# Performance work log

Hardware: AMD Instinct MI355X
Metric: run time of the kernel (lower is better)

## Reference

```python
import jax, jax.numpy as jnp
import numpy as np

D_MODEL = 1024
N_HEADS = 16
D_V = D_MODEL // N_HEADS  # 64


def setup_inputs() -> dict:
    key = jax.random.key(0)
    k1, k2, k3, k4, k5, k6 = jax.random.split(key, 6)
    N, L = 2, 2048
    return {
        "queries": jax.random.normal(k1, (N, L, D_MODEL), jnp.float32),
        "keys": jax.random.normal(k2, (N, L, D_MODEL), jnp.float32),
        "values": jax.random.normal(k3, (N, L, D_MODEL), jnp.float32),
        # key-padding mask, 0 = masked out (broadcast over heads and queries)
        "mask": jax.random.randint(k4, (N, 1, 1, L), 0, 2).astype(jnp.int32),
        # torch nn.Linear(d_model, d_model): weight [out, in], bias [out]
        "fc_w": jax.random.normal(k5, (D_MODEL, D_MODEL), jnp.float32) / np.sqrt(D_MODEL).astype(np.float32),
        "fc_b": jax.random.normal(k6, (D_MODEL,), jnp.float32) * 0.01,
    }


def reference(queries, keys, values, mask, fc_w, fc_b):
    N, Lq, _ = queries.shape
    Lk = keys.shape[1]
    # NOTE: the source defines Q/K/V Linear layers but never applies them in forward.
    q = queries.reshape(N, Lq, N_HEADS, D_V).transpose(0, 2, 1, 3)  # [N,H,Lq,Dv]
    k = keys.reshape(N, Lk, N_HEADS, D_V)                            # [N,Lk,H,Dv]
    v = values.reshape(N, Lk, N_HEADS, D_V)                          # [N,Lk,H,Dv]
    energy = jnp.einsum('nhqd,nkhd->nhqk', q, k)                     # QK^T
    energy = jnp.where(mask == 0, -jnp.inf, energy)                  # masked_fill
    # faithful to source: scale by sqrt(d_model), applied after masking
    attn = jax.nn.softmax(energy / jnp.sqrt(jnp.float32(D_MODEL)), axis=-1)
    out = jnp.einsum('nhqk,nkhd->nqhd', attn, v).reshape(N, Lq, N_HEADS * D_V)
    return out @ fc_w.T + fc_b
```

## Files before the change

kernel.cpp:

```cpp
#include <hip/hip_runtime.h>
#include <hip/hip_bf16.h>

#define SEQL 2048
#define DMODEL 1024

typedef short bf16x8 __attribute__((ext_vector_type(8)));
typedef short bf16x4 __attribute__((ext_vector_type(4)));
typedef float f32x4 __attribute__((ext_vector_type(4)));
typedef unsigned short u16;

__device__ __forceinline__ u16 f2bf(float f) {
    union { float f; unsigned u; } v; v.f = f;
    unsigned r = v.u + 0x7FFFu + ((v.u >> 16) & 1u);
    return (u16)(r >> 16);
}

#define TSTR 66

__global__ __launch_bounds__(256) void pack_all(
    const float* __restrict__ kg, const float* __restrict__ wg,
    const float* __restrict__ vg, const int* __restrict__ mg,
    u16* __restrict__ kb, u16* __restrict__ wb, u16* __restrict__ vtb,
    float* __restrict__ maskf)
{
    __shared__ __align__(16) u16 T[64 * TSTR];
    const int b = blockIdx.x, t = threadIdx.x;
    u16 o[8];
    if (b < 2048) {
        const int e0 = (b * 256 + t) * 8;
        const int n = e0 >> 21, rem = e0 & ((1 << 21) - 1);
        const int s = rem >> 10, dm = rem & 1023, h = dm >> 6, d = dm & 63;
        const float4 x0 = *(const float4*)(kg + e0);
        const float4 x1 = *(const float4*)(kg + e0 + 4);
        o[0]=f2bf(x0.x); o[1]=f2bf(x0.y); o[2]=f2bf(x0.z); o[3]=f2bf(x0.w);
        o[4]=f2bf(x1.x); o[5]=f2bf(x1.y); o[6]=f2bf(x1.z); o[7]=f2bf(x1.w);
        *(bf16x8*)(kb + ((((size_t)n * 16 + h) * 2048 + s) * 64 + d)) = *(bf16x8*)o;
    } else if (b < 2560) {
        const int e0 = ((b - 2048) * 256 + t) * 8;
        const float4 x0 = *(const float4*)(wg + e0);
        const float4 x1 = *(const float4*)(wg + e0 + 4);
        o[0]=f2bf(x0.x); o[1]=f2bf(x0.y); o[2]=f2bf(x0.z); o[3]=f2bf(x0.w);
        o[4]=f2bf(x1.x); o[5]=f2bf(x1.y); o[6]=f2bf(x1.z); o[7]=f2bf(x1.w);
        *(bf16x8*)(wb + e0) = *(bf16x8*)o;
    } else if (b < 3584) {
        const int bb = b - 2560;
        const int st = bb & 31, h = (bb >> 5) & 15, n = bb >> 9;
        {
            const int s = t >> 2, d0 = (t & 3) * 16;
            const float* src = vg + ((size_t)(n * SEQL + st * 64 + s) * DMODEL) + h * 64 + d0;
            u16 w16[16];
            #pragma unroll
            for (int j = 0; j < 16; ++j) w16[j] = f2bf(src[j]);
            *(bf16x8*)&T[s * TSTR + d0]     = *(bf16x8*)&w16[0];
            *(bf16x8*)&T[s * TSTR + d0 + 8] = *(bf16x8*)&w16[8];
        }
        __syncthreads();
        {
            const int d = t >> 2, k0 = (t & 3) * 16;
            u16 w16[16];
            #pragma unroll
            for (int j = 0; j < 16; ++j) w16[j] = T[(k0 + j) * TSTR + d];
            u16* dst = vtb + ((size_t)((n * 16 + h) * 64 + d) * SEQL) + st * 64 + k0;
            *(bf16x8*)dst       = *(bf16x8*)&w16[0];
            *(bf16x8*)(dst + 8) = *(bf16x8*)&w16[8];
        }
    } else {
        #pragma unroll
        for (int i = 0; i < 16; ++i) {
            const int idx = t * 16 + i;
            maskf[idx] = mg[idx] ? 0.0f : -1.0e5f;
        }
    }
}

#define KSTR 66
#define VSTR 66
#define PT 66
#define OSPLIT 4194304
#define LSPLIT 65536

template<int NSPLIT>
__global__ __launch_bounds__(256) void attn_kernel(
    const float* __restrict__ qg, const u16* __restrict__ kb,
    const u16* __restrict__ vtb, const float* __restrict__ maskf,
    u16* __restrict__ xb, float* __restrict__ opart, float* __restrict__ lpart)
{
    __shared__ __align__(16) u16 K_lds[64 * KSTR];
    __shared__ __align__(16) u16 Vt_lds[64 * VSTR];
    __shared__ __align__(16) u16 P_lds[128 * PT];

    const int blk = blockIdx.x;
    const int qblk = blk & 15;
    const int h = (blk >> 4) & 15;
    const int n = (blk >> 8) & 1;
    const int split = blk >> 9;
    const int tid = threadIdx.x;
    const int wave = tid >> 6, lane = tid & 63;
    const int lrow = lane & 15, quad = lane >> 4;
    const int q0 = qblk * 128;

    bf16x8 qf[2][2];
    #pragma unroll
    for (int qi = 0; qi < 2; ++qi) {
        const float* qp = qg + ((size_t)(n * SEQL + q0 + wave * 32 + qi * 16 + lrow) * DMODEL) + h * 64 + quad * 8;
        #pragma unroll
        for (int f = 0; f < 2; ++f) {
            const float4 a = *(const float4*)(qp + f * 32);
            const float4 c = *(const float4*)(qp + f * 32 + 4);
            u16* dst = (u16*)&qf[qi][f];
            dst[0]=f2bf(a.x); dst[1]=f2bf(a.y); dst[2]=f2bf(a.z); dst[3]=f2bf(a.w);
            dst[4]=f2bf(c.x); dst[5]=f2bf(c.y); dst[6]=f2bf(c.z); dst[7]=f2bf(c.w);
        }
    }

    bf16x8 onesf;
    #pragma unroll
    for (int j = 0; j < 8; ++j) ((u16*)&onesf)[j] = 0x3F80;

    f32x4 oacc[2][4];
    f32x4 lacc[2];
    #pragma unroll
    for (int qi = 0; qi < 2; ++qi) {
        lacc[qi] = (f32x4){0.f, 0.f, 0.f, 0.f};
        #pragma unroll
        for (int t4 = 0; t4 < 4; ++t4) oacc[qi][t4] = (f32x4){0.f, 0.f, 0.f, 0.f};
    }

    const u16* ksrc0 = kb  + ((size_t)(n * 16 + h) * SEQL) * 64;
    const u16* vsrc0 = vtb + ((size_t)(n * 16 + h) * 64) * SEQL;
    const float* mrow = maskf + n * SEQL;

    const int ktlo = split * (32 / NSPLIT);
    const int kthi = ktlo + (32 / NSPLIT);

    for (int kt = ktlo; kt < kthi; ++kt) {
        __syncthreads();
        {
            const u16* ks = ksrc0 + (size_t)kt * 64 * 64;
            const u16* vs = vsrc0 + kt * 64;
            #pragma unroll
            for (int i = 0; i < 2; ++i) {
                const int c = tid + i * 256;
                const int r = c >> 3, e0 = (c & 7) * 8;
                *(bf16x8*)&K_lds[r * KSTR + e0]  = *(const bf16x8*)(ks + c * 8);
                *(bf16x8*)&Vt_lds[r * VSTR + e0] = *(const bf16x8*)(vs + (size_t)r * SEQL + e0);
            }
        }
        __syncthreads();

        #pragma unroll
        for (int st = 0; st < 4; ++st) {
            const bf16x8 kf0 = *(const bf16x8*)&K_lds[(st * 16 + lrow) * KSTR + quad * 8];
            const bf16x8 kf1 = *(const bf16x8*)&K_lds[(st * 16 + lrow) * KSTR + 32 + quad * 8];
            const f32x4 mv = *(const f32x4*)&mrow[kt * 64 + st * 16 + quad * 4];
            #pragma unroll
            for (int qi = 0; qi < 2; ++qi) {
                f32x4 sa = (f32x4){0.f, 0.f, 0.f, 0.f};
                sa = __builtin_amdgcn_mfma_f32_16x16x32_bf16(kf0, qf[qi][0], sa, 0, 0, 0);
                sa = __builtin_amdgcn_mfma_f32_16x16x32_bf16(kf1, qf[qi][1], sa, 0, 0, 0);
                float e0v = __expf(fmaf(sa[0], 0.03125f, mv[0]));
                float e1v = __expf(fmaf(sa[1], 0.03125f, mv[1]));
                float e2v = __expf(fmaf(sa[2], 0.03125f, mv[2]));
                float e3v = __expf(fmaf(sa[3], 0.03125f, mv[3]));
                __hip_bfloat162 h0 = __float22bfloat162_rn(make_float2(e0v, e1v));
                __hip_bfloat162 h1 = __float22bfloat162_rn(make_float2(e2v, e3v));
                union { unsigned u[2]; bf16x4 v; } pk;
                pk.u[0] = *(unsigned*)&h0;
                pk.u[1] = *(unsigned*)&h1;
                *(bf16x4*)&P_lds[(wave * 32 + qi * 16 + lrow) * PT + st * 16 + quad * 4] = pk.v;
            }
        }
        asm volatile("s_waitcnt lgkmcnt(0)" ::: "memory");

        bf16x8 vf[4][2];
        #pragma unroll
        for (int t4 = 0; t4 < 4; ++t4) {
            vf[t4][0] = *(const bf16x8*)&Vt_lds[(t4 * 16 + lrow) * VSTR + quad * 8];
            vf[t4][1] = *(const bf16x8*)&Vt_lds[(t4 * 16 + lrow) * VSTR + 32 + quad * 8];
        }
        #pragma unroll
        for (int qi = 0; qi < 2; ++qi) {
            const int prow = (wave * 32 + qi * 16 + lrow) * PT;
            const bf16x8 pf0 = *(const bf16x8*)&P_lds[prow + quad * 8];
            const bf16x8 pf1 = *(const bf16x8*)&P_lds[prow + 32 + quad * 8];
            lacc[qi] = __builtin_amdgcn_mfma_f32_16x16x32_bf16(pf0, onesf, lacc[qi], 0, 0, 0);
            lacc[qi] = __builtin_amdgcn_mfma_f32_16x16x32_bf16(pf1, onesf, lacc[qi], 0, 0, 0);
            #pragma unroll
            for (int t4 = 0; t4 < 4; ++t4) {
                oacc[qi][t4] = __builtin_amdgcn_mfma_f32_16x16x32_bf16(pf0, vf[t4][0], oacc[qi][t4], 0, 0, 0);
                oacc[qi][t4] = __builtin_amdgcn_mfma_f32_16x16x32_bf16(pf1, vf[t4][1], oacc[qi][t4], 0, 0, 0);
            }
        }
    }

    if (NSPLIT == 1) {
        #pragma unroll
        for (int qi = 0; qi < 2; ++qi)
            #pragma unroll
            for (int r = 0; r < 4; ++r) {
                const float rinv = 1.0f / lacc[qi][r];
                const int q = q0 + wave * 32 + qi * 16 + quad * 4 + r;
                u16* op = xb + (size_t)(n * SEQL + q) * DMODEL + h * 64 + lrow;
                #pragma unroll
                for (int t4 = 0; t4 < 4; ++t4)
                    op[t4 * 16] = f2bf(oacc[qi][t4][r] * rinv);
            }
    } else {
        #pragma unroll
        for (int qi = 0; qi < 2; ++qi) {
            #pragma unroll
            for (int r = 0; r < 4; ++r) {
                const int q = q0 + wave * 32 + qi * 16 + quad * 4 + r;
                float* op = opart + (size_t)split * OSPLIT + (size_t)(n * SEQL + q) * DMODEL + h * 64 + lrow;
                #pragma unroll
                for (int t4 = 0; t4 < 4; ++t4)
                    op[t4 * 16] = oacc[qi][t4][r];
                if (lrow == 0)
                    lpart[split * LSPLIT + (n * SEQL + q) * 16 + h] = lacc[qi][r];
            }
        }
    }
}

template<int NSPLIT>
__global__ __launch_bounds__(256) void reduce_norm(
    const float* __restrict__ opart, const float* __restrict__ lpart,
    u16* __restrict__ xb)
{
    const int gid = blockIdx.x * 256 + threadIdx.x;
    const int e0 = gid * 8;
    const int row = e0 >> 10, c = e0 & 1023, h = c >> 6;
    float lsum = 0.f;
    #pragma unroll
    for (int s = 0; s < NSPLIT; ++s) lsum += lpart[s * LSPLIT + row * 16 + h];
    const float rinv = 1.0f / lsum;
    float a[8] = {0.f,0.f,0.f,0.f,0.f,0.f,0.f,0.f};
    #pragma unroll
    for (int s = 0; s < NSPLIT; ++s) {
        const float4 x0 = *(const float4*)(opart + (size_t)s * OSPLIT + e0);
        const float4 x1 = *(const float4*)(opart + (size_t)s * OSPLIT + e0 + 4);
        a[0]+=x0.x; a[1]+=x0.y; a[2]+=x0.z; a[3]+=x0.w;
        a[4]+=x1.x; a[5]+=x1.y; a[6]+=x1.z; a[7]+=x1.w;
    }
    u16 o[8];
    #pragma unroll
    for (int j = 0; j < 8; ++j) o[j] = f2bf(a[j] * rinv);
    *(bf16x8*)(xb + e0) = *(bf16x8*)o;
}

#define FSTR 66

__global__ __launch_bounds__(256) void fc_kernel(
    const u16* __restrict__ xb, const u16* __restrict__ wb,
    const float* __restrict__ bias, float* __restrict__ out)
{
    __shared__ __align__(16) u16 X_lds[128 * FSTR];
    __shared__ __align__(16) u16 W_lds[64 * FSTR];

    const int blk = blockIdx.x;
    const int cb = blk & 15, rb = blk >> 4;
    const int row0 = rb * 128, col0 = cb * 64;
    const int tid = threadIdx.x;
    const int wave = tid >> 6, lane = tid & 63;
    const int lrow = lane & 15, quad = lane >> 4;

    f32x4 acc[2][4];
    #pragma unroll
    for (int ri = 0; ri < 2; ++ri)
        #pragma unroll
        for (int cj = 0; cj < 4; ++cj) acc[ri][cj] = (f32x4){0.f, 0.f, 0.f, 0.f};

    for (int kt = 0; kt < 16; ++kt) {
        __syncthreads();
        #pragma unroll
        for (int i = 0; i < 4; ++i) {
            const int g = tid + i * 256;
            const int r = g >> 3, e0 = (g & 7) * 8;
            *(bf16x8*)&X_lds[r * FSTR + e0] =
                *(const bf16x8*)(xb + (size_t)(row0 + r) * DMODEL + kt * 64 + e0);
        }
        #pragma unroll
        for (int i = 0; i < 2; ++i) {
            const int g = tid + i * 256;
            const int r = g >> 3, e0 = (g & 7) * 8;
            *(bf16x8*)&W_lds[r * FSTR + e0] =
                *(const bf16x8*)(wb + (size_t)(col0 + r) * DMODEL + kt * 64 + e0);
        }
        __syncthreads();

        bf16x8 af[2][2];
        #pragma unroll
        for (int ri = 0; ri < 2; ++ri) {
            af[ri][0] = *(const bf16x8*)&X_lds[(wave * 32 + ri * 16 + lrow) * FSTR + quad * 8];
            af[ri][1] = *(const bf16x8*)&X_lds[(wave * 32 + ri * 16 + lrow) * FSTR + 32 + quad * 8];
        }
        #pragma unroll
        for (int cj = 0; cj < 4; ++cj) {
            const bf16x8 bf0 = *(const bf16x8*)&W_lds[(cj * 16 + lrow) * FSTR + quad * 8];
            const bf16x8 bf1 = *(const bf16x8*)&W_lds[(cj * 16 + lrow) * FSTR + 32 + quad * 8];
            #pragma unroll
            for (int ri = 0; ri < 2; ++ri) {
                acc[ri][cj] = __builtin_amdgcn_mfma_f32_16x16x32_bf16(af[ri][0], bf0, acc[ri][cj], 0, 0, 0);
                acc[ri][cj] = __builtin_amdgcn_mfma_f32_16x16x32_bf16(af[ri][1], bf1, acc[ri][cj], 0, 0, 0);
            }
        }
    }

    #pragma unroll
    for (int ri = 0; ri < 2; ++ri)
        #pragma unroll
        for (int cj = 0; cj < 4; ++cj) {
            const int col = col0 + cj * 16 + lrow;
            const float bv = bias[col];
            #pragma unroll
            for (int r = 0; r < 4; ++r)
                out[(size_t)(row0 + wave * 32 + ri * 16 + quad * 4 + r) * DMODEL + col] = acc[ri][cj][r] + bv;
        }
}

extern "C" void kernel_launch(void* const* d_in, const int* in_sizes, int n_in,
                              void* d_out, int out_size, void* d_ws, size_t ws_size,
                              hipStream_t stream) {
    const float* q   = (const float*)d_in[0];
    const float* k   = (const float*)d_in[1];
    const float* v   = (const float*)d_in[2];
    const int*   m   = (const int*)d_in[3];
    const float* fcw = (const float*)d_in[4];
    const float* fcb = (const float*)d_in[5];
    float* out = (float*)d_out;

    char* ws = (char*)d_ws;
    u16*   kbuf  = (u16*)(ws);
    u16*   vtbuf = (u16*)(ws + (8u  << 20));
    u16*   wbuf  = (u16*)(ws + (16u << 20));
    u16*   xbuf  = (u16*)(ws + (18u << 20));
    float* maskf = (float*)(ws + (26u << 20));
    float* opart = (float*)(ws + (27u << 20));
    const bool split4 = ws_size >= (93u << 20);
    const bool split2 = ws_size >= (60u << 20);

    pack_all<<<dim3(3585), dim3(256), 0, stream>>>(k, fcw, v, m, kbuf, wbuf, vtbuf, maskf);
    if (split4) {
        float* lpart = (float*)(ws + (91u << 20));
        attn_kernel<4><<<dim3(2048), dim3(256), 0, stream>>>(q, kbuf, vtbuf, maskf, xbuf, opart, lpart);
        reduce_norm<4><<<dim3(2048), dim3(256), 0, stream>>>(opart, lpart, xbuf);
    } else if (split2) {
        float* lpart = (float*)(ws + (59u << 20));
        attn_kernel<2><<<dim3(1024), dim3(256), 0, stream>>>(q, kbuf, vtbuf, maskf, xbuf, opart, lpart);
        reduce_norm<2><<<dim3(2048), dim3(256), 0, stream>>>(opart, lpart, xbuf);
    } else {
        float* lpart = (float*)(ws + (59u << 20));
        attn_kernel<1><<<dim3(512), dim3(256), 0, stream>>>(q, kbuf, vtbuf, maskf, xbuf, opart, lpart);
    }
    fc_kernel<<<dim3(512), dim3(256), 0, stream>>>(xbuf, wbuf, fcb, out);
}
```

Baseline: 210.2 us.

## Pre-swizzle K, V, W, X into MFMA fragment layout and load tiles via LDS DMA

The pack kernel and the attention epilogue and reduce kernel now write K, V^T, W and the attention output in a fragment-major layout that matches the 16x16x32 MFMA operand order. Tiles can then be copied straight into LDS with global_load_lds 16-byte async loads, and each lane reads its fragment contiguously at lane*8, with no padded strides. The P buffer uses the same fragment layout. The 4-way key split path is removed, so the 2-way split is used when workspace allows. This is meant to cut LDS bank conflicts and VGPR staging on tile loads, at the cost of more complex scattered writes in the pack and epilogue stages and fewer blocks in attention.

```diff
diff --git a/kernel.cpp b/kernel.cpp
--- a/kernel.cpp
+++ b/kernel.cpp
@@ -15,7 +15,15 @@
     return (u16)(r >> 16);
 }
 
-#define TSTR 66
+__device__ __forceinline__ void async16(u16* lds, const u16* g) {
+    __builtin_amdgcn_global_load_lds(
+        (const __attribute__((address_space(1))) unsigned int*)g,
+        (__attribute__((address_space(3))) unsigned int*)lds,
+        16, 0, 0);
+}
+
+
+#define TSTR 72
 
 __global__ __launch_bounds__(256) void pack_all(
     const float* __restrict__ kg, const float* __restrict__ wg,
@@ -28,26 +36,36 @@
     u16 o[8];
     if (b < 2048) {
         const int e0 = (b * 256 + t) * 8;
-        const int n = e0 >> 21, rem = e0 & ((1 << 21) - 1);
-        const int s = rem >> 10, dm = rem & 1023, h = dm >> 6, d = dm & 63;
+        const int n = e0 >> 21;
+        const int s = (e0 >> 10) & 2047;
+        const int dm = e0 & 1023, h = dm >> 6, d0 = dm & 63;
         const float4 x0 = *(const float4*)(kg + e0);
         const float4 x1 = *(const float4*)(kg + e0 + 4);
         o[0]=f2bf(x0.x); o[1]=f2bf(x0.y); o[2]=f2bf(x0.z); o[3]=f2bf(x0.w);
         o[4]=f2bf(x1.x); o[5]=f2bf(x1.y); o[6]=f2bf(x1.z); o[7]=f2bf(x1.w);
-        *(bf16x8*)(kb + ((((size_t)n * 16 + h) * 2048 + s) * 64 + d)) = *(bf16x8*)o;
+        const int kt = s >> 6, st = (s >> 4) & 3, m = s & 15;
+        const int f = d0 >> 5, qd = (d0 >> 3) & 3;
+        u16* dst = kb + ((size_t)((n * 16 + h) * 32 + kt)) * 4096
+                      + (st * 2 + f) * 512 + (m + 16 * qd) * 8;
+        *(bf16x8*)dst = *(bf16x8*)o;
     } else if (b < 2560) {
         const int e0 = ((b - 2048) * 256 + t) * 8;
+        const int col = e0 >> 10, k0 = e0 & 1023;
         const float4 x0 = *(const float4*)(wg + e0);
         const float4 x1 = *(const float4*)(wg + e0 + 4);
         o[0]=f2bf(x0.x); o[1]=f2bf(x0.y); o[2]=f2bf(x0.z); o[3]=f2bf(x0.w);
         o[4]=f2bf(x1.x); o[5]=f2bf(x1.y); o[6]=f2bf(x1.z); o[7]=f2bf(x1.w);
-        *(bf16x8*)(wb + e0) = *(bf16x8*)o;
+        const int cb = col >> 6, cj = (col >> 4) & 3, m = col & 15;
+        const int kt = k0 >> 6, f = (k0 >> 5) & 1, qd = (k0 >> 3) & 3;
+        u16* dst = wb + ((size_t)((cb * 16 + kt) * 8 + cj * 2 + f)) * 512
+                      + (m + 16 * qd) * 8;
+        *(bf16x8*)dst = *(bf16x8*)o;
     } else if (b < 3584) {
         const int bb = b - 2560;
-        const int st = bb & 31, h = (bb >> 5) & 15, n = bb >> 9;
+        const int kt = bb & 31, h = (bb >> 5) & 15, n = bb >> 9;
         {
             const int s = t >> 2, d0 = (t & 3) * 16;
-            const float* src = vg + ((size_t)(n * SEQL + st * 64 + s) * DMODEL) + h * 64 + d0;
+            const float* src = vg + ((size_t)(n * SEQL + kt * 64 + s) * DMODEL) + h * 64 + d0;
             u16 w16[16];
             #pragma unroll
             for (int j = 0; j < 16; ++j) w16[j] = f2bf(src[j]);
@@ -60,9 +78,15 @@
             u16 w16[16];
             #pragma unroll
             for (int j = 0; j < 16; ++j) w16[j] = T[(k0 + j) * TSTR + d];
-            u16* dst = vtb + ((size_t)((n * 16 + h) * 64 + d) * SEQL) + st * 64 + k0;
-            *(bf16x8*)dst       = *(bf16x8*)&w16[0];
-            *(bf16x8*)(dst + 8) = *(bf16x8*)&w16[8];
+            const int t4 = d >> 4, dr = d & 15;
+            u16* base = vtb + ((size_t)((n * 16 + h) * 32 + kt)) * 4096;
+            #pragma unroll
+            for (int g = 0; g < 2; ++g) {
+                const int key0 = k0 + g * 8;
+                const int kk = key0 >> 5, qk = (key0 >> 3) & 3;
+                *(bf16x8*)(base + (t4 * 2 + kk) * 512 + (dr + 16 * qk) * 8)
+                    = *(bf16x8*)&w16[g * 8];
+            }
         }
     } else {
         #pragma unroll
@@ -73,9 +97,6 @@
     }
 }
 
-#define KSTR 66
-#define VSTR 66
-#define PT 66
 #define OSPLIT 4194304
 #define LSPLIT 65536
 
@@ -85,9 +106,10 @@
     const u16* __restrict__ vtb, const float* __restrict__ maskf,
     u16* __restrict__ xb, float* __restrict__ opart, float* __restrict__ lpart)
 {
-    __shared__ __align__(16) u16 K_lds[64 * KSTR];
-    __shared__ __align__(16) u16 Vt_lds[64 * VSTR];
-    __shared__ __align__(16) u16 P_lds[128 * PT];
+    __shared__ __align__(16) u16 SM[16384];
+    u16* const K_lds = SM;
+    u16* const V_lds = SM + 4096;
+    u16* const P_lds = SM + 8192;
 
     const int blk = blockIdx.x;
     const int qblk = blk & 15;
@@ -126,8 +148,8 @@
         for (int t4 = 0; t4 < 4; ++t4) oacc[qi][t4] = (f32x4){0.f, 0.f, 0.f, 0.f};
     }
 
-    const u16* ksrc0 = kb  + ((size_t)(n * 16 + h) * SEQL) * 64;
-    const u16* vsrc0 = vtb + ((size_t)(n * 16 + h) * 64) * SEQL;
+    const u16* ksrc0 = kb  + ((size_t)(n * 16 + h)) * 131072;
+    const u16* vsrc0 = vtb + ((size_t)(n * 16 + h)) * 131072;
     const float* mrow = maskf + n * SEQL;
 
     const int ktlo = split * (32 / NSPLIT);
@@ -136,23 +158,25 @@
     for (int kt = ktlo; kt < kthi; ++kt) {
         __syncthreads();
         {
-            const u16* ks = ksrc0 + (size_t)kt * 64 * 64;
-            const u16* vs = vsrc0 + kt * 64;
+            const u16* ks = ksrc0 + (size_t)kt * 4096;
+            const u16* vs = vsrc0 + (size_t)kt * 4096;
             #pragma unroll
             for (int i = 0; i < 2; ++i) {
-                const int c = tid + i * 256;
-                const int r = c >> 3, e0 = (c & 7) * 8;
-                *(bf16x8*)&K_lds[r * KSTR + e0]  = *(const bf16x8*)(ks + c * 8);
-                *(bf16x8*)&Vt_lds[r * VSTR + e0] = *(const bf16x8*)(vs + (size_t)r * SEQL + e0);
+                const int ch = tid + i * 256;
+                async16(&K_lds[ch * 8], ks + ch * 8);
+                async16(&V_lds[ch * 8], vs + ch * 8);
             }
         }
         __syncthreads();
 
         #pragma unroll
         for (int st = 0; st < 4; ++st) {
-            const bf16x8 kf0 = *(const bf16x8*)&K_lds[(st * 16 + lrow) * KSTR + quad * 8];
-            const bf16x8 kf1 = *(const bf16x8*)&K_lds[(st * 16 + lrow) * KSTR + 32 + quad * 8];
+            const bf16x8 kf0 = *(const bf16x8*)&K_lds[(st * 2 + 0) * 512 + lane * 8];
+            const bf16x8 kf1 = *(const bf16x8*)&K_lds[(st * 2 + 1) * 512 + lane * 8];
             const f32x4 mv = *(const f32x4*)&mrow[kt * 64 + st * 16 + quad * 4];
+            const int kk = st >> 1;
+            const int qk = (st & 1) * 2 + (quad >> 1);
+            const int j0 = (quad & 1) * 4;
             #pragma unroll
             for (int qi = 0; qi < 2; ++qi) {
                 f32x4 sa = (f32x4){0.f, 0.f, 0.f, 0.f};
@@ -167,7 +191,7 @@
                 union { unsigned u[2]; bf16x4 v; } pk;
                 pk.u[0] = *(unsigned*)&h0;
                 pk.u[1] = *(unsigned*)&h1;
-                *(bf16x4*)&P_lds[(wave * 32 + qi * 16 + lrow) * PT + st * 16 + quad * 4] = pk.v;
+                *(bf16x4*)&P_lds[wave * 2048 + (qi * 2 + kk) * 512 + (lrow + 16 * qk) * 8 + j0] = pk.v;
             }
         }
         asm volatile("s_waitcnt lgkmcnt(0)" ::: "memory");
@@ -175,14 +199,13 @@
         bf16x8 vf[4][2];
         #pragma unroll
         for (int t4 = 0; t4 < 4; ++t4) {
-            vf[t4][0] = *(const bf16x8*)&Vt_lds[(t4 * 16 + lrow) * VSTR + quad * 8];
-            vf[t4][1] = *(const bf16x8*)&Vt_lds[(t4 * 16 + lrow) * VSTR + 32 + quad * 8];
+            vf[t4][0] = *(const bf16x8*)&V_lds[(t4 * 2 + 0) * 512 + lane * 8];
+            vf[t4][1] = *(const bf16x8*)&V_lds[(t4 * 2 + 1) * 512 + lane * 8];
         }
         #pragma unroll
         for (int qi = 0; qi < 2; ++qi) {
-            const int prow = (wave * 32 + qi * 16 + lrow) * PT;
-            const bf16x8 pf0 = *(const bf16x8*)&P_lds[prow + quad * 8];
-            const bf16x8 pf1 = *(const bf16x8*)&P_lds[prow + 32 + quad * 8];
+            const bf16x8 pf0 = *(const bf16x8*)&P_lds[wave * 2048 + (qi * 2 + 0) * 512 + lane * 8];
+            const bf16x8 pf1 = *(const bf16x8*)&P_lds[wave * 2048 + (qi * 2 + 1) * 512 + lane * 8];
             lacc[qi] = __builtin_amdgcn_mfma_f32_16x16x32_bf16(pf0, onesf, lacc[qi], 0, 0, 0);
             lacc[qi] = __builtin_amdgcn_mfma_f32_16x16x32_bf16(pf1, onesf, lacc[qi], 0, 0, 0);
             #pragma unroll
@@ -199,11 +222,15 @@
             #pragma unroll
             for (int r = 0; r < 4; ++r) {
                 const float rinv = 1.0f / lacc[qi][r];
-                const int q = q0 + wave * 32 + qi * 16 + quad * 4 + r;
-                u16* op = xb + (size_t)(n * SEQL + q) * DMODEL + h * 64 + lrow;
+                const int row = n * SEQL + q0 + wave * 32 + qi * 16 + quad * 4 + r;
+                const int rb = row >> 7, rt = (row >> 4) & 7, m = row & 15;
                 #pragma unroll
-                for (int t4 = 0; t4 < 4; ++t4)
-                    op[t4 * 16] = f2bf(oacc[qi][t4][r] * rinv);
+                for (int t4 = 0; t4 < 4; ++t4) {
+                    const int f = t4 >> 1;
+                    const int qd = (t4 & 1) * 2 + (lrow >> 3);
+                    xb[((size_t)((rb * 16 + h) * 16 + rt * 2 + f)) * 512
+                       + (m + 16 * qd) * 8 + (lrow & 7)] = f2bf(oacc[qi][t4][r] * rinv);
+                }
             }
     } else {
         #pragma unroll
@@ -229,7 +256,7 @@
 {
     const int gid = blockIdx.x * 256 + threadIdx.x;
     const int e0 = gid * 8;
-    const int row = e0 >> 10, c = e0 & 1023, h = c >> 6;
+    const int row = e0 >> 10, k0 = e0 & 1023, h = k0 >> 6;
     float lsum = 0.f;
     #pragma unroll
     for (int s = 0; s < NSPLIT; ++s) lsum += lpart[s * LSPLIT + row * 16 + h];
@@ -245,21 +272,22 @@
     u16 o[8];
     #pragma unroll
     for (int j = 0; j < 8; ++j) o[j] = f2bf(a[j] * rinv);
-    *(bf16x8*)(xb + e0) = *(bf16x8*)o;
-}
-
-#define FSTR 66
+    const int rb = row >> 7, rt = (row >> 4) & 7, m = row & 15;
+    const int kt = k0 >> 6, f = (k0 >> 5) & 1, qd = (k0 >> 3) & 3;
+    *(bf16x8*)(xb + ((size_t)((rb * 16 + kt) * 16 + rt * 2 + f)) * 512
+                  + (m + 16 * qd) * 8) = *(bf16x8*)o;
+}
 
 __global__ __launch_bounds__(256) void fc_kernel(
     const u16* __restrict__ xb, const u16* __restrict__ wb,
     const float* __restrict__ bias, float* __restrict__ out)
 {
-    __shared__ __align__(16) u16 X_lds[128 * FSTR];
-    __shared__ __align__(16) u16 W_lds[64 * FSTR];
+    __shared__ __align__(16) u16 SM[12288];
+    u16* const X_lds = SM;
+    u16* const W_lds = SM + 8192;
 
     const int blk = blockIdx.x;
     const int cb = blk & 15, rb = blk >> 4;
-    const int row0 = rb * 128, col0 = cb * 64;
     const int tid = threadIdx.x;
     const int wave = tid >> 6, lane = tid & 63;
     const int lrow = lane & 15, quad = lane >> 4;
@@ -272,32 +300,32 @@
 
     for (int kt = 0; kt < 16; ++kt) {
         __syncthreads();
-        #pragma unroll
-        for (int i = 0; i < 4; ++i) {
-            const int g = tid + i * 256;
-            const int r = g >> 3, e0 = (g & 7) * 8;
-            *(bf16x8*)&X_lds[r * FSTR + e0] =
-                *(const bf16x8*)(xb + (size_t)(row0 + r) * DMODEL + kt * 64 + e0);
-        }
-        #pragma unroll
-        for (int i = 0; i < 2; ++i) {
-            const int g = tid + i * 256;
-            const int r = g >> 3, e0 = (g & 7) * 8;
-            *(bf16x8*)&W_lds[r * FSTR + e0] =
-                *(const bf16x8*)(wb + (size_t)(col0 + r) * DMODEL + kt * 64 + e0);
+        {
+            const u16* xs = xb + ((size_t)(rb * 16 + kt)) * 8192;
+            const u16* ws = wb + ((size_t)(cb * 16 + kt)) * 4096;
+            #pragma unroll
+            for (int i = 0; i < 4; ++i) {
+                const int ch = tid + i * 256;
+                async16(&X_lds[ch * 8], xs + ch * 8);
+            }
+            #pragma unroll
+            for (int i = 0; i < 2; ++i) {
+                const int ch = tid + i * 256;
+                async16(&W_lds[ch * 8], ws + ch * 8);
+            }
         }
         __syncthreads();
 
         bf16x8 af[2][2];
         #pragma unroll
         for (int ri = 0; ri < 2; ++ri) {
-            af[ri][0] = *(const bf16x8*)&X_lds[(wave * 32 + ri * 16 + lrow) * FSTR + quad * 8];
-            af[ri][1] = *(const bf16x8*)&X_lds[(wave * 32 + ri * 16 + lrow) * FSTR + 32 + quad * 8];
+            af[ri][0] = *(const bf16x8*)&X_lds[((wave * 2 + ri) * 2 + 0) * 512 + lane * 8];
+            af[ri][1] = *(const bf16x8*)&X_lds[((wave * 2 + ri) * 2 + 1) * 512 + lane * 8];
         }
         #pragma unroll
         for (int cj = 0; cj < 4; ++cj) {
-            const bf16x8 bf0 = *(const bf16x8*)&W_lds[(cj * 16 + lrow) * FSTR + quad * 8];
-            const bf16x8 bf1 = *(const bf16x8*)&W_lds[(cj * 16 + lrow) * FSTR + 32 + quad * 8];
+            const bf16x8 bf0 = *(const bf16x8*)&W_lds[(cj * 2 + 0) * 512 + lane * 8];
+            const bf16x8 bf1 = *(const bf16x8*)&W_lds[(cj * 2 + 1) * 512 + lane * 8];
             #pragma unroll
             for (int ri = 0; ri < 2; ++ri) {
                 acc[ri][cj] = __builtin_amdgcn_mfma_f32_16x16x32_bf16(af[ri][0], bf0, acc[ri][cj], 0, 0, 0);
@@ -306,6 +334,7 @@
         }
     }
 
+    const int row0 = rb * 128, col0 = cb * 64;
     #pragma unroll
     for (int ri = 0; ri < 2; ++ri)
         #pragma unroll
@@ -336,20 +365,14 @@
     u16*   xbuf  = (u16*)(ws + (18u << 20));
     float* maskf = (float*)(ws + (26u << 20));
     float* opart = (float*)(ws + (27u << 20));
-    const bool split4 = ws_size >= (93u << 20);
+    float* lpart = (float*)(ws + (59u << 20));
     const bool split2 = ws_size >= (60u << 20);
 
     pack_all<<<dim3(3585), dim3(256), 0, stream>>>(k, fcw, v, m, kbuf, wbuf, vtbuf, maskf);
-    if (split4) {
-        float* lpart = (float*)(ws + (91u << 20));
-        attn_kernel<4><<<dim3(2048), dim3(256), 0, stream>>>(q, kbuf, vtbuf, maskf, xbuf, opart, lpart);
-        reduce_norm<4><<<dim3(2048), dim3(256), 0, stream>>>(opart, lpart, xbuf);
-    } else if (split2) {
-        float* lpart = (float*)(ws + (59u << 20));
+    if (split2) {
         attn_kernel<2><<<dim3(1024), dim3(256), 0, stream>>>(q, kbuf, vtbuf, maskf, xbuf, opart, lpart);
         reduce_norm<2><<<dim3(2048), dim3(256), 0, stream>>>(opart, lpart, xbuf);
     } else {
-        float* lpart = (float*)(ws + (59u << 20));
         attn_kernel<1><<<dim3(512), dim3(256), 0, stream>>>(q, kbuf, vtbuf, maskf, xbuf, opart, lpart);
     }
     fc_kernel<<<dim3(512), dim3(256), 0, stream>>>(xbuf, wbuf, fcb, out);
```

Result: faster. 179.0 us (-14.8%).
